# Kernel optimization log

Measured on AMD Instinct MI355X. Metric: run time of the kernel, lower is better.

The kernel has to match this reference:

```python
import jax, jax.numpy as jnp
import numpy as np

H, D = 16, 64            # heads_num, mouse_hidden_dim // heads_num
START_FRAME = 9728       # current_start (token units)
GLOBAL_END_PREV = 9728   # kv_cache['global_end_index'] before this call
LOCAL_END_PREV = 9728    # kv_cache['local_end_index'] before this call
SINK = 0                 # sink_tokens in source
WINDOW = 8192            # max_attention_size = local_attn_size (token units)


def _rope_interleaved(x, cos_h, sin_h):
    # non-neox (interleaved) rotary: x [B,S,H,D], cos_h/sin_h [S, D//2]
    x1 = x[..., 0::2]
    x2 = x[..., 1::2]
    c = cos_h[None, :, None, :]
    s = sin_h[None, :, None, :]
    o1 = x1 * c - x2 * s
    o2 = x2 * c + x1 * s
    return jnp.stack([o1, o2], axis=-1).reshape(x.shape)


def setup_inputs() -> dict:
    key = jax.random.key(0)
    ks = jax.random.split(key, 7)
    B, S, C = 1, 1024, 10240
    return {
        'q': jax.random.normal(ks[0], (B, S, H, D), jnp.float32),
        'k': jax.random.normal(ks[1], (B, S, H, D), jnp.float32),
        'v': jax.random.normal(ks[2], (B, S, H, D), jnp.float32),
        'cache_k': jax.random.normal(ks[3], (B, C, H, D), jnp.float32),
        'cache_v': jax.random.normal(ks[4], (B, C, H, D), jnp.float32),
        'freqs_cos': jax.random.uniform(ks[5], (START_FRAME + S, D), jnp.float32, -1.0, 1.0),
        'freqs_sin': jax.random.uniform(ks[6], (START_FRAME + S, D), jnp.float32, -1.0, 1.0),
    }


def reference(q, k, v, cache_k, cache_v, freqs_cos, freqs_sin):
    B, S, _, _ = q.shape
    # _apply_rotary_emb_qk: slice freqs at start_offset, take every-other col (cos_half)
    cos_h = freqs_cos[START_FRAME:START_FRAME + S, ::2]  # [S, D//2]
    sin_h = freqs_sin[START_FRAME:START_FRAME + S, ::2]
    q_r = _rope_interleaved(q, cos_h, sin_h)
    k_r = _rope_interleaved(k, cos_h, sin_h)

    # ring-buffer KV-cache update (all index math is static Python ints)
    current_end = START_FRAME + S
    cache_size = cache_k.shape[1]
    num_new = S
    if current_end > GLOBAL_END_PREV and num_new + LOCAL_END_PREV > cache_size:
        num_evicted = num_new + LOCAL_END_PREV - cache_size
        num_rolled = LOCAL_END_PREV - num_evicted - SINK
        rolled_k = jax.lax.dynamic_slice_in_dim(cache_k, SINK + num_evicted, num_rolled, axis=1)
        rolled_v = jax.lax.dynamic_slice_in_dim(cache_v, SINK + num_evicted, num_rolled, axis=1)
        cache_k = cache_k.at[:, SINK:SINK + num_rolled].set(rolled_k)
        cache_v = cache_v.at[:, SINK:SINK + num_rolled].set(rolled_v)
        local_end = LOCAL_END_PREV + current_end - GLOBAL_END_PREV - num_evicted
    else:
        local_end = LOCAL_END_PREV + current_end - GLOBAL_END_PREV
    local_start = local_end - num_new
    cache_k = cache_k.at[:, local_start:local_end].set(k_r)
    cache_v = cache_v.at[:, local_start:local_end].set(v)

    # windowed (last local_attn_size tokens) non-causal attention
    cache_start = max(0, local_end - WINDOW)
    wk = cache_k[:, cache_start:local_end]  # [B, W, H, D]
    wv = cache_v[:, cache_start:local_end]
    scale = 1.0 / np.float32(np.sqrt(D))
    scores = jnp.einsum('bqhd,bkhd->bhqk', q_r, wk) * scale
    probs = jax.nn.softmax(scores, axis=-1)
    out = jnp.einsum('bhqk,bkhd->bqhd', probs, wv)
    return out.reshape(B, S, H * D)
```

## Files before the change

kernel.cpp:

```cpp
#include <hip/hip_runtime.h>

#define HH 16
#define DD 64
#define SQ 1024
#define LW 8192
#define OLDK 7168
#define CACHE_BASE 2560
#define SFRAME 9728
#define KSPLIT 8
#define KPER (LW / KSPLIT)
#define NSTEP (KPER / 64)

#define KB_OFF 0u
#define VT_OFF 16777216u
#define QB_OFF 33554432u
#define OP_OFF 35651584u
#define LP_OFF 69206016u

typedef __bf16 bf16x8 __attribute__((ext_vector_type(8)));
typedef float floatx16 __attribute__((ext_vector_type(16)));
typedef unsigned uintx2 __attribute__((ext_vector_type(2)));
typedef unsigned uintx4 __attribute__((ext_vector_type(4)));

__device__ __forceinline__ unsigned short f2bf(float f) {
  unsigned u = __builtin_bit_cast(unsigned, f);
  u += 0x7fffu + ((u >> 16) & 1u);
  return (unsigned short)(u >> 16);
}

__device__ __forceinline__ float fast_exp2(float x) {
#if __has_builtin(__builtin_amdgcn_exp2f)
  return __builtin_amdgcn_exp2f(x);
#else
  return __builtin_exp2f(x);
#endif
}

__device__ __forceinline__ unsigned pack_bf2(float a, float b) {
#if __has_builtin(__builtin_amdgcn_cvt_pk_bf16_f32)
  typedef __bf16 bf16x2_t __attribute__((ext_vector_type(2)));
  bf16x2_t r = __builtin_amdgcn_cvt_pk_bf16_f32(a, b);
  return __builtin_bit_cast(unsigned, r);
#else
  unsigned ua = __builtin_bit_cast(unsigned, a) + 0x8000u;
  unsigned ub = __builtin_bit_cast(unsigned, b) + 0x8000u;
  return __builtin_amdgcn_perm(ub, ua, 0x07060302);
#endif
}

__device__ __forceinline__ void async16(void* lds, const void* g) {
  __builtin_amdgcn_global_load_lds((__attribute__((address_space(1))) void*)(g),
                                   (__attribute__((address_space(3))) void*)(lds),
                                   16, 0, 0);
}

__global__ __launch_bounds__(256) void prepass(
    const float* __restrict__ qin, const float* __restrict__ kin,
    const float* __restrict__ vin, const float* __restrict__ ck,
    const float* __restrict__ cv, const float* __restrict__ fc,
    const float* __restrict__ fs, unsigned short* __restrict__ Kb,
    unsigned short* __restrict__ Vt, unsigned short* __restrict__ Qb) {
  int b = blockIdx.x, t = threadIdx.x;
  if (b < 1024) {
    __shared__ float tl[128 * 64];
    int h = b >> 6, kk0 = (b & 63) * 128;
    int c = t & 15;
#pragma unroll
    for (int it = 0; it < 8; it++) {
      int kk = it * 16 + (t >> 4);
      int gk = kk0 + kk;
      const float* src = (gk < OLDK)
                             ? cv + (CACHE_BASE + gk) * (HH * DD) + h * DD + 4 * c
                             : vin + (gk - OLDK) * (HH * DD) + h * DD + 4 * c;
      float4 vv = *(const float4*)src;
      int cg = c ^ (kk >> 3);
      *(float4*)(tl + kk * 64 + cg * 4) = vv;
    }
    __syncthreads();
    int kq = t & 15;
#pragma unroll
    for (int jt = 0; jt < 4; jt++) {
      int d = jt * 16 + (t >> 4);
      ushort4 lo, hi;
      unsigned short tmp[8];
#pragma unroll
      for (int j = 0; j < 8; j++) {
        int kk = 8 * kq + j;
        int cg = (d >> 2) ^ kq;
        tmp[j] = f2bf(tl[kk * 64 + cg * 4 + (d & 3)]);
      }
      lo.x = tmp[0]; lo.y = tmp[1]; lo.z = tmp[2]; lo.w = tmp[3];
      hi.x = tmp[4]; hi.y = tmp[5]; hi.z = tmp[6]; hi.w = tmp[7];
      unsigned short* dst = Vt + (h * DD + d) * LW + kk0 + 8 * kq;
      *(ushort4*)(dst) = lo;
      *(ushort4*)(dst + 4) = hi;
    }
  } else if (b < 8192) {
    int b1 = b - 1024;
    int h = b1 / 448, g = b1 % 448;
    int kk = g * 16 + (t >> 4);
    int lane = t & 15;
    float4 val = *(const float4*)(ck + (CACHE_BASE + kk) * (HH * DD) + h * DD + lane * 4);
    ushort4 o;
    o.x = f2bf(val.x); o.y = f2bf(val.y); o.z = f2bf(val.z); o.w = f2bf(val.w);
    *(ushort4*)(Kb + (h * LW + kk) * DD + lane * 4) = o;
  } else if (b < 10240) {
    int b2 = b - 8192;
    int rh = b2 * 8 + (t >> 5);
    int s = rh >> 4, h = rh & 15, i = t & 31;
    float2 x = *(const float2*)(kin + s * (HH * DD) + h * DD + 2 * i);
    float c = fc[(SFRAME + s) * DD + 2 * i];
    float sn = fs[(SFRAME + s) * DD + 2 * i];
    ushort2 o;
    o.x = f2bf(x.x * c - x.y * sn);
    o.y = f2bf(x.y * c + x.x * sn);
    *(ushort2*)(Kb + (h * LW + OLDK + s) * DD + 2 * i) = o;
  } else {
    int b3 = b - 10240;
    int rh = b3 * 8 + (t >> 5);
    int s = rh >> 4, h = rh & 15, i = t & 31;
    const float SC = 0.18033688011112042f;
    float2 x = *(const float2*)(qin + s * (HH * DD) + h * DD + 2 * i);
    float c = fc[(SFRAME + s) * DD + 2 * i];
    float sn = fs[(SFRAME + s) * DD + 2 * i];
    ushort2 o;
    o.x = f2bf((x.x * c - x.y * sn) * SC);
    o.y = f2bf((x.y * c + x.x * sn) * SC);
    *(ushort2*)(Qb + (h * SQ + s) * DD + 2 * i) = o;
  }
}

__global__ __launch_bounds__(256, 2) void attn(
    const unsigned short* __restrict__ Kb, const unsigned short* __restrict__ Vt,
    const unsigned short* __restrict__ Qb, unsigned short* __restrict__ Op,
    float* __restrict__ Lp) {
  __shared__ __align__(16) unsigned char sK[2][8192];
  __shared__ __align__(16) unsigned char sV[2][8192];

  int bid = blockIdx.x;
  int g = bid & 127, qb = bid >> 7;
  int h = g & 15, ks = g >> 4;
  int t = threadIdx.x;
  int w = t >> 6, lane = t & 63;
  int l31 = lane & 31, e = lane >> 5;
  int q0 = qb * 256 + w * 64;

  int baseA = (l31 & 7) ^ ((l31 >> 3) & 7);
  int baseB = (l31 & 7) ^ (((l31 >> 3) + 4) & 7);

  bf16x8 qf[2][4];
#pragma unroll
  for (int tq = 0; tq < 2; tq++) {
    const unsigned short* qptr = Qb + (h * SQ + q0 + 32 * tq + l31) * DD + 8 * e;
#pragma unroll
    for (int c = 0; c < 4; c++) qf[tq][c] = *(const bf16x8*)(qptr + 16 * c);
  }

  floatx16 o[2][2];
#pragma unroll
  for (int a = 0; a < 2; a++)
#pragma unroll
    for (int bb = 0; bb < 2; bb++)
#pragma unroll
      for (int i = 0; i < 16; i++) o[a][bb][i] = 0.f;
  float ls[2] = {0.f, 0.f};

  const unsigned short* KbH = Kb + h * (LW * DD);
  const unsigned short* VtH = Vt + h * (DD * LW);
  int kkBase = ks * KPER;

  auto stage = [&](int buf, int kk0) {
#pragma unroll
    for (int hf = 0; hf < 2; hf++) {
      int gi = w * 128 + hf * 64 + lane;
      int rr = gi >> 3;
      int src = (gi & 7) ^ (rr & 7) ^ ((rr >> 3) & 7);
      async16(sK[buf] + gi * 16, KbH + (kk0 + rr) * DD + src * 8);
      async16(sV[buf] + gi * 16, VtH + rr * LW + kk0 + src * 8);
    }
  };

  auto softmax_half = [&](floatx16& sv, int tq, int tk, bf16x8 pf[2][4]) {
#pragma unroll
    for (int i = 0; i < 16; i++) sv[i] = fast_exp2(sv[i]);
    float p0 = (sv[0] + sv[1]) + (sv[2] + sv[3]);
    float p1 = (sv[4] + sv[5]) + (sv[6] + sv[7]);
    float p2 = (sv[8] + sv[9]) + (sv[10] + sv[11]);
    float p3 = (sv[12] + sv[13]) + (sv[14] + sv[15]);
    ls[tq] += (p0 + p1) + (p2 + p3);
#pragma unroll
    for (int kcp = 0; kcp < 2; kcp++) {
      unsigned u0 = pack_bf2(sv[8 * kcp + 0], sv[8 * kcp + 1]);
      unsigned u1 = pack_bf2(sv[8 * kcp + 2], sv[8 * kcp + 3]);
      unsigned u2 = pack_bf2(sv[8 * kcp + 4], sv[8 * kcp + 5]);
      unsigned u3 = pack_bf2(sv[8 * kcp + 6], sv[8 * kcp + 7]);
      uintx2 r0 = __builtin_amdgcn_permlane32_swap(u0, u2, false, false);
      uintx2 r1 = __builtin_amdgcn_permlane32_swap(u1, u3, false, false);
      uintx4 f;
      f[0] = r0[0]; f[1] = r1[0]; f[2] = r0[1]; f[3] = r1[1];
      pf[tq][2 * tk + kcp] = __builtin_bit_cast(bf16x8, f);
    }
  };

  stage(0, kkBase);

  for (int st = 0; st < NSTEP; st++) {
    __syncthreads();
    if (st + 1 < NSTEP) stage((st + 1) & 1, kkBase + (st + 1) * 64);
    const unsigned char* cK = sK[st & 1];
    const unsigned char* cV = sV[st & 1];

    bf16x8 pf[2][4];

    floatx16 sA0, sA1;
#pragma unroll
    for (int i = 0; i < 16; i++) { sA0[i] = 0.f; sA1[i] = 0.f; }
#pragma unroll
    for (int c = 0; c < 4; c++) {
      int p = (2 * c + e) ^ baseA;
      bf16x8 ka = *(const bf16x8*)(cK + (l31 * 8 + p) * 16);
      sA0 = __builtin_amdgcn_mfma_f32_32x32x16_bf16(ka, qf[0][c], sA0, 0, 0, 0);
      sA1 = __builtin_amdgcn_mfma_f32_32x32x16_bf16(ka, qf[1][c], sA1, 0, 0, 0);
    }

    floatx16 sB0, sB1;
#pragma unroll
    for (int i = 0; i < 16; i++) { sB0[i] = 0.f; sB1[i] = 0.f; }
#pragma unroll
    for (int c = 0; c < 4; c++) {
      int p = (2 * c + e) ^ baseB;
      bf16x8 kb = *(const bf16x8*)(cK + ((l31 + 32) * 8 + p) * 16);
      sB0 = __builtin_amdgcn_mfma_f32_32x32x16_bf16(kb, qf[0][c], sB0, 0, 0, 0);
      sB1 = __builtin_amdgcn_mfma_f32_32x32x16_bf16(kb, qf[1][c], sB1, 0, 0, 0);
    }

    softmax_half(sA0, 0, 0, pf);
    softmax_half(sA1, 1, 0, pf);

#pragma unroll
    for (int kc = 0; kc < 2; kc++) {
      int pA = (2 * kc + e) ^ baseA;
      int pB = (2 * kc + e) ^ baseB;
      bf16x8 va = *(const bf16x8*)(cV + (l31 * 8 + pA) * 16);
      bf16x8 vb = *(const bf16x8*)(cV + ((l31 + 32) * 8 + pB) * 16);
      o[0][0] = __builtin_amdgcn_mfma_f32_32x32x16_bf16(va, pf[0][kc], o[0][0], 0, 0, 0);
      o[0][1] = __builtin_amdgcn_mfma_f32_32x32x16_bf16(vb, pf[0][kc], o[0][1], 0, 0, 0);
      o[1][0] = __builtin_amdgcn_mfma_f32_32x32x16_bf16(va, pf[1][kc], o[1][0], 0, 0, 0);
      o[1][1] = __builtin_amdgcn_mfma_f32_32x32x16_bf16(vb, pf[1][kc], o[1][1], 0, 0, 0);
    }

    softmax_half(sB0, 0, 1, pf);
    softmax_half(sB1, 1, 1, pf);

#pragma unroll
    for (int kc = 2; kc < 4; kc++) {
      int pA = (2 * kc + e) ^ baseA;
      int pB = (2 * kc + e) ^ baseB;
      bf16x8 va = *(const bf16x8*)(cV + (l31 * 8 + pA) * 16);
      bf16x8 vb = *(const bf16x8*)(cV + ((l31 + 32) * 8 + pB) * 16);
      o[0][0] = __builtin_amdgcn_mfma_f32_32x32x16_bf16(va, pf[0][kc], o[0][0], 0, 0, 0);
      o[0][1] = __builtin_amdgcn_mfma_f32_32x32x16_bf16(vb, pf[0][kc], o[0][1], 0, 0, 0);
      o[1][0] = __builtin_amdgcn_mfma_f32_32x32x16_bf16(va, pf[1][kc], o[1][0], 0, 0, 0);
      o[1][1] = __builtin_amdgcn_mfma_f32_32x32x16_bf16(vb, pf[1][kc], o[1][1], 0, 0, 0);
    }
  }

#pragma unroll
  for (int tq = 0; tq < 2; tq++) {
    float l = ls[tq];
    l += __shfl_xor(l, 32, 64);
    int qrow = q0 + 32 * tq + l31;
    unsigned short* op = Op + (((ks * 16 + h) * SQ) + qrow) * DD;
#pragma unroll
    for (int t4 = 0; t4 < 4; t4++) {
      uint2 a, b;
      a.x = pack_bf2(o[tq][0][4 * t4 + 0], o[tq][0][4 * t4 + 1]);
      a.y = pack_bf2(o[tq][0][4 * t4 + 2], o[tq][0][4 * t4 + 3]);
      b.x = pack_bf2(o[tq][1][4 * t4 + 0], o[tq][1][4 * t4 + 1]);
      b.y = pack_bf2(o[tq][1][4 * t4 + 2], o[tq][1][4 * t4 + 3]);
      *(uint2*)(op + 8 * t4 + 4 * e) = a;
      *(uint2*)(op + 32 + 8 * t4 + 4 * e) = b;
    }
    if (e == 0) Lp[(ks * 16 + h) * SQ + qrow] = l;
  }
}

__global__ __launch_bounds__(256) void combine(const unsigned short* __restrict__ Op,
                                               const float* __restrict__ Lp,
                                               float* __restrict__ out) {
  int idx = blockIdx.x * 256 + threadIdx.x;
  int d4 = idx & 15, q = (idx >> 4) & 1023, h = idx >> 14;
  float num[4] = {0.f, 0.f, 0.f, 0.f};
  float den = 0.f;
#pragma unroll
  for (int s = 0; s < KSPLIT; s++) {
    int row = (s * 16 + h) * SQ + q;
    uint2 pkv = *(const uint2*)(Op + row * DD + 4 * d4);
    num[0] += __builtin_bit_cast(float, pkv.x << 16);
    num[1] += __builtin_bit_cast(float, pkv.x & 0xffff0000u);
    num[2] += __builtin_bit_cast(float, pkv.y << 16);
    num[3] += __builtin_bit_cast(float, pkv.y & 0xffff0000u);
    den += Lp[row];
  }
  float r = 1.0f / den;
  float4 ov;
  ov.x = num[0] * r; ov.y = num[1] * r; ov.z = num[2] * r; ov.w = num[3] * r;
  *(float4*)(out + q * (HH * DD) + h * DD + 4 * d4) = ov;
}

extern "C" void kernel_launch(void* const* d_in, const int* in_sizes, int n_in,
                              void* d_out, int out_size, void* d_ws, size_t ws_size,
                              hipStream_t stream) {
  const float* q  = (const float*)d_in[0];
  const float* k  = (const float*)d_in[1];
  const float* v  = (const float*)d_in[2];
  const float* ck = (const float*)d_in[3];
  const float* cv = (const float*)d_in[4];
  const float* fc = (const float*)d_in[5];
  const float* fs = (const float*)d_in[6];
  float* out = (float*)d_out;
  char* ws = (char*)d_ws;

  unsigned short* Kb = (unsigned short*)(ws + KB_OFF);
  unsigned short* Vt = (unsigned short*)(ws + VT_OFF);
  unsigned short* Qb = (unsigned short*)(ws + QB_OFF);
  unsigned short* Op = (unsigned short*)(ws + OP_OFF);
  float* Lp = (float*)(ws + LP_OFF);

  prepass<<<12288, 256, 0, stream>>>(q, k, v, ck, cv, fc, fs, Kb, Vt, Qb);
  attn<<<512, 256, 0, stream>>>(Kb, Vt, Qb, Op, Lp);
  combine<<<1024, 256, 0, stream>>>(Op, Lp, out);
}
```

Baseline: 179.8 us.

## Pad V transpose tile, packed softmax sums, zero-init MFMA, delay next-stage prefetch

The V-transpose prepass drops the XOR swizzle and uses a 65-float row pitch in shared memory. In the attention loop, the row sums switch to two-wide float vectors so packed adds can be used, and the first MFMA of each score block takes a constant zero accumulator instead of zeroing registers. The async prefetch of the next K/V stage now issues after the first QK MFMA block instead of right after the barrier, so it overlaps compute differently. The padded pitch breaks 16-byte alignment of the float4 stores into the tile, and issuing the prefetch later gives the loads less time to land before the next iteration.

```diff
diff --git a/kernel.cpp b/kernel.cpp
--- a/kernel.cpp
+++ b/kernel.cpp
@@ -19,6 +19,7 @@
 
 typedef __bf16 bf16x8 __attribute__((ext_vector_type(8)));
 typedef float floatx16 __attribute__((ext_vector_type(16)));
+typedef float floatx2 __attribute__((ext_vector_type(2)));
 typedef unsigned uintx2 __attribute__((ext_vector_type(2)));
 typedef unsigned uintx4 __attribute__((ext_vector_type(4)));
 
@@ -62,7 +63,7 @@
     unsigned short* __restrict__ Vt, unsigned short* __restrict__ Qb) {
   int b = blockIdx.x, t = threadIdx.x;
   if (b < 1024) {
-    __shared__ float tl[128 * 64];
+    __shared__ float tl[128 * 65];
     int h = b >> 6, kk0 = (b & 63) * 128;
     int c = t & 15;
 #pragma unroll
@@ -73,8 +74,7 @@
                              ? cv + (CACHE_BASE + gk) * (HH * DD) + h * DD + 4 * c
                              : vin + (gk - OLDK) * (HH * DD) + h * DD + 4 * c;
       float4 vv = *(const float4*)src;
-      int cg = c ^ (kk >> 3);
-      *(float4*)(tl + kk * 64 + cg * 4) = vv;
+      *(float4*)(tl + kk * 65 + c * 4) = vv;
     }
     __syncthreads();
     int kq = t & 15;
@@ -86,8 +86,7 @@
 #pragma unroll
       for (int j = 0; j < 8; j++) {
         int kk = 8 * kq + j;
-        int cg = (d >> 2) ^ kq;
-        tmp[j] = f2bf(tl[kk * 64 + cg * 4 + (d & 3)]);
+        tmp[j] = f2bf(tl[kk * 65 + d]);
       }
       lo.x = tmp[0]; lo.y = tmp[1]; lo.z = tmp[2]; lo.w = tmp[3];
       hi.x = tmp[4]; hi.y = tmp[5]; hi.z = tmp[6]; hi.w = tmp[7];
@@ -165,6 +164,8 @@
       for (int i = 0; i < 16; i++) o[a][bb][i] = 0.f;
   float ls[2] = {0.f, 0.f};
 
+  const floatx16 fz = {0.f};
+
   const unsigned short* KbH = Kb + h * (LW * DD);
   const unsigned short* VtH = Vt + h * (DD * LW);
   int kkBase = ks * KPER;
@@ -183,19 +184,29 @@
   auto softmax_half = [&](floatx16& sv, int tq, int tk, bf16x8 pf[2][4]) {
 #pragma unroll
     for (int i = 0; i < 16; i++) sv[i] = fast_exp2(sv[i]);
-    float p0 = (sv[0] + sv[1]) + (sv[2] + sv[3]);
-    float p1 = (sv[4] + sv[5]) + (sv[6] + sv[7]);
-    float p2 = (sv[8] + sv[9]) + (sv[10] + sv[11]);
-    float p3 = (sv[12] + sv[13]) + (sv[14] + sv[15]);
-    ls[tq] += (p0 + p1) + (p2 + p3);
+    floatx2 t0, t1, t2, t3;
+    t0[0] = sv[0];  t0[1] = sv[1];
+    t1[0] = sv[2];  t1[1] = sv[3];
+    t2[0] = sv[4];  t2[1] = sv[5];
+    t3[0] = sv[6];  t3[1] = sv[7];
+    floatx2 u0 = t0 + t1, u1 = t2 + t3;
+    floatx2 t4, t5, t6, t7;
+    t4[0] = sv[8];  t4[1] = sv[9];
+    t5[0] = sv[10]; t5[1] = sv[11];
+    t6[0] = sv[12]; t6[1] = sv[13];
+    t7[0] = sv[14]; t7[1] = sv[15];
+    floatx2 u2 = t4 + t5, u3 = t6 + t7;
+    floatx2 v0 = u0 + u1, v1 = u2 + u3;
+    floatx2 vs = v0 + v1;
+    ls[tq] += vs[0] + vs[1];
 #pragma unroll
     for (int kcp = 0; kcp < 2; kcp++) {
-      unsigned u0 = pack_bf2(sv[8 * kcp + 0], sv[8 * kcp + 1]);
-      unsigned u1 = pack_bf2(sv[8 * kcp + 2], sv[8 * kcp + 3]);
-      unsigned u2 = pack_bf2(sv[8 * kcp + 4], sv[8 * kcp + 5]);
-      unsigned u3 = pack_bf2(sv[8 * kcp + 6], sv[8 * kcp + 7]);
-      uintx2 r0 = __builtin_amdgcn_permlane32_swap(u0, u2, false, false);
-      uintx2 r1 = __builtin_amdgcn_permlane32_swap(u1, u3, false, false);
+      unsigned u0p = pack_bf2(sv[8 * kcp + 0], sv[8 * kcp + 1]);
+      unsigned u1p = pack_bf2(sv[8 * kcp + 2], sv[8 * kcp + 3]);
+      unsigned u2p = pack_bf2(sv[8 * kcp + 4], sv[8 * kcp + 5]);
+      unsigned u3p = pack_bf2(sv[8 * kcp + 6], sv[8 * kcp + 7]);
+      uintx2 r0 = __builtin_amdgcn_permlane32_swap(u0p, u2p, false, false);
+      uintx2 r1 = __builtin_amdgcn_permlane32_swap(u1p, u3p, false, false);
       uintx4 f;
       f[0] = r0[0]; f[1] = r1[0]; f[2] = r0[1]; f[3] = r1[1];
       pf[tq][2 * tk + kcp] = __builtin_bit_cast(bf16x8, f);
@@ -206,32 +217,41 @@
 
   for (int st = 0; st < NSTEP; st++) {
     __syncthreads();
-    if (st + 1 < NSTEP) stage((st + 1) & 1, kkBase + (st + 1) * 64);
     const unsigned char* cK = sK[st & 1];
     const unsigned char* cV = sV[st & 1];
 
     bf16x8 pf[2][4];
 
     floatx16 sA0, sA1;
-#pragma unroll
-    for (int i = 0; i < 16; i++) { sA0[i] = 0.f; sA1[i] = 0.f; }
-#pragma unroll
-    for (int c = 0; c < 4; c++) {
-      int p = (2 * c + e) ^ baseA;
-      bf16x8 ka = *(const bf16x8*)(cK + (l31 * 8 + p) * 16);
-      sA0 = __builtin_amdgcn_mfma_f32_32x32x16_bf16(ka, qf[0][c], sA0, 0, 0, 0);
-      sA1 = __builtin_amdgcn_mfma_f32_32x32x16_bf16(ka, qf[1][c], sA1, 0, 0, 0);
-    }
+    {
+      int p0 = e ^ baseA;
+      bf16x8 ka0 = *(const bf16x8*)(cK + (l31 * 8 + p0) * 16);
+      sA0 = __builtin_amdgcn_mfma_f32_32x32x16_bf16(ka0, qf[0][0], fz, 0, 0, 0);
+      sA1 = __builtin_amdgcn_mfma_f32_32x32x16_bf16(ka0, qf[1][0], fz, 0, 0, 0);
+#pragma unroll
+      for (int c = 1; c < 4; c++) {
+        int p = (2 * c + e) ^ baseA;
+        bf16x8 ka = *(const bf16x8*)(cK + (l31 * 8 + p) * 16);
+        sA0 = __builtin_amdgcn_mfma_f32_32x32x16_bf16(ka, qf[0][c], sA0, 0, 0, 0);
+        sA1 = __builtin_amdgcn_mfma_f32_32x32x16_bf16(ka, qf[1][c], sA1, 0, 0, 0);
+      }
+    }
+
+    if (st + 1 < NSTEP) stage((st + 1) & 1, kkBase + (st + 1) * 64);
 
     floatx16 sB0, sB1;
-#pragma unroll
-    for (int i = 0; i < 16; i++) { sB0[i] = 0.f; sB1[i] = 0.f; }
-#pragma unroll
-    for (int c = 0; c < 4; c++) {
-      int p = (2 * c + e) ^ baseB;
-      bf16x8 kb = *(const bf16x8*)(cK + ((l31 + 32) * 8 + p) * 16);
-      sB0 = __builtin_amdgcn_mfma_f32_32x32x16_bf16(kb, qf[0][c], sB0, 0, 0, 0);
-      sB1 = __builtin_amdgcn_mfma_f32_32x32x16_bf16(kb, qf[1][c], sB1, 0, 0, 0);
+    {
+      int p0 = e ^ baseB;
+      bf16x8 kb0 = *(const bf16x8*)(cK + ((l31 + 32) * 8 + p0) * 16);
+      sB0 = __builtin_amdgcn_mfma_f32_32x32x16_bf16(kb0, qf[0][0], fz, 0, 0, 0);
+      sB1 = __builtin_amdgcn_mfma_f32_32x32x16_bf16(kb0, qf[1][0], fz, 0, 0, 0);
+#pragma unroll
+      for (int c = 1; c < 4; c++) {
+        int p = (2 * c + e) ^ baseB;
+        bf16x8 kb = *(const bf16x8*)(cK + ((l31 + 32) * 8 + p) * 16);
+        sB0 = __builtin_amdgcn_mfma_f32_32x32x16_bf16(kb, qf[0][c], sB0, 0, 0, 0);
+        sB1 = __builtin_amdgcn_mfma_f32_32x32x16_bf16(kb, qf[1][c], sB1, 0, 0, 0);
+      }
     }
 
     softmax_half(sA0, 0, 0, pf);
```

After: 177.9 us. About the same (-1.1%).
